# Kernel optimization log

Hardware: AMD Instinct MI355X
Metric: run time of the kernel (lower is better)

Reference implementation:

```python
import jax, jax.numpy as jnp
import numpy as np
import math

B, S, D_MODEL, HEADS, HK = 1024, 81, 64, 4, 16  # S=81 from dim1=5184/64; HK=head dim
FFN, LAYERS, NCLS = 128, 2, 16
EPS = 1e-5


def setup_inputs() -> dict:
    key = jax.random.key(0)
    ks = iter(jax.random.split(key, 40))
    def rn(shape, scale=1.0):
        return jax.random.normal(next(ks), shape, jnp.float32) * scale
    d = {}
    d['X'] = rn((B, 1, 30, 13, 13))
    d['c3w'] = rn((8, 1, 3, 3, 3), 0.1); d['c3b'] = jnp.zeros((8,), jnp.float32)
    d['bn3g'] = jnp.ones((8,), jnp.float32); d['bn3b'] = jnp.zeros((8,), jnp.float32)
    d['c2w'] = rn((64, 224, 3, 3), 0.05); d['c2b'] = jnp.zeros((64,), jnp.float32)
    d['bn2g'] = jnp.ones((64,), jnp.float32); d['bn2b'] = jnp.zeros((64,), jnp.float32)
    d['wq'] = rn((LAYERS, HEADS, D_MODEL, HK), 1.0 / D_MODEL)
    d['wk'] = rn((LAYERS, HEADS, D_MODEL, HK), 1.0 / D_MODEL)
    d['wv'] = rn((LAYERS, HEADS, D_MODEL, HK), 1.0 / D_MODEL)
    d['wg'] = rn((LAYERS, D_MODEL, D_MODEL), 1.0 / D_MODEL)
    d['wo'] = rn((LAYERS, D_MODEL, D_MODEL), 1.0 / D_MODEL)
    d['gng'] = jnp.ones((LAYERS, D_MODEL), jnp.float32); d['gnb'] = jnp.zeros((LAYERS, D_MODEL), jnp.float32)
    d['ln1g'] = jnp.ones((LAYERS, D_MODEL), jnp.float32); d['ln1b'] = jnp.zeros((LAYERS, D_MODEL), jnp.float32)
    d['ln2g'] = jnp.ones((LAYERS, D_MODEL), jnp.float32); d['ln2b'] = jnp.zeros((LAYERS, D_MODEL), jnp.float32)
    d['fw1'] = rn((LAYERS, D_MODEL, FFN), 0.05); d['fb1'] = jnp.zeros((LAYERS, FFN), jnp.float32)
    d['fw2'] = rn((LAYERS, FFN, D_MODEL), 0.05); d['fb2'] = jnp.zeros((LAYERS, D_MODEL), jnp.float32)
    d['nn1w'] = rn((S * D_MODEL, NCLS), 0.02); d['nn1b'] = rn((NCLS,), 1e-6)
    return d


def _bn(x, g, b, axes):
    # BatchNorm in training mode (module default): batch statistics, biased var
    mu = x.mean(axes, keepdims=True)
    var = x.var(axes, keepdims=True)
    shp = [1] * x.ndim; shp[1] = -1
    return (x - mu) / jnp.sqrt(var + EPS) * g.reshape(shp) + b.reshape(shp)


def _ln(x, g, b):
    mu = x.mean(-1, keepdims=True)
    var = x.var(-1, keepdims=True)
    return (x - mu) / jnp.sqrt(var + EPS) * g + b


def _rot2(x):
    # rotate_every_two: (x0,x1,x2,x3,...) -> (-x1,x0,-x3,x2,...)
    x1, x2 = x[..., ::2], x[..., 1::2]
    return jnp.stack((-x2, x1), axis=-1).reshape(x.shape)


def _xpos_tables():
    scale = (jnp.arange(0, HK, 2, dtype=jnp.float32) + 0.4 * HK) / (1.4 * HK)  # (HK/2,)
    pos = jnp.arange(S, dtype=jnp.float32)
    xs = scale[None, :] ** (pos[:, None] / 512.0)                               # (S, HK/2)
    inv_freq = 1.0 / (10000.0 ** (jnp.arange(HK // 2, dtype=jnp.float32) / (HK // 2)))
    ang = pos[:, None] * inv_freq[None, :]
    sin, cos = jnp.sin(ang), jnp.cos(ang)
    dup = lambda m: jnp.repeat(m, 2, axis=-1)                                   # (S, HK)
    return dup(cos * xs), dup(sin * xs), dup(cos / xs), dup(sin / xs)


def _decay_mask():
    g = 1.0 - jnp.exp(jnp.linspace(math.log(1 / 32), math.log(1 / 512), HEADS))
    nm = jnp.arange(S)[:, None] - jnp.arange(S)[None, :]
    return jnp.where(nm >= 0, g[:, None, None] ** nm, 0.0)                      # (H,S,S)


def _forward(X, c3w, c3b, bn3g, bn3b, c2w, c2b, bn2g, bn2b,
             wq, wk, wv, wg, wo, gng, gnb, ln1g, ln1b, ln2g, ln2b,
             fw1, fb1, fw2, fb2, nn1w, nn1b):
    # Convnet front-end
    x = jax.lax.conv_general_dilated(X, c3w, (1, 1, 1), 'VALID',
                                     dimension_numbers=('NCDHW', 'OIDHW', 'NCDHW'))
    x = x + c3b[None, :, None, None, None]
    x = jax.nn.relu(_bn(x, bn3g, bn3b, (0, 2, 3, 4)))        # (B,8,28,11,11)
    x = x.reshape(B, 8 * 28, 11, 11)                           # 'b c h w y -> b (c h) w y'
    x = jax.lax.conv_general_dilated(x, c2w, (1, 1), 'VALID',
                                     dimension_numbers=('NCHW', 'OIHW', 'NCHW'))
    x = x + c2b[None, :, None, None]
    x = jax.nn.relu(_bn(x, bn2g, bn2b, (0, 2, 3)))           # (B,64,9,9)
    x = x.transpose(0, 2, 3, 1).reshape(B, S, D_MODEL)        # 'b c h w -> b (h w) c'

    cu, su, cd, sd = _xpos_tables()
    Dm = _decay_mask()
    for l in range(LAYERS):
        h = _ln(x, ln1g[l], ln1b[l])
        # per-head retention (parallel form)
        Q = jnp.einsum('bsd,hdk->bhsk', h, wq[l])
        K = jnp.einsum('bsd,hdk->bhsk', h, wk[l])
        V = jnp.einsum('bsd,hdk->bhsk', h, wv[l])
        Q = Q * cu + _rot2(Q) * su                            # xpos upscale
        K = K * cd + _rot2(K) * sd                            # xpos downscale
        att = jnp.einsum('bhsk,bhtk->bhst', Q, K) * Dm[None]  # decay-masked scores
        Yh = jnp.einsum('bhst,bhtv->bhsv', att, V)            # (B,H,S,HK)
        # GroupNorm(heads, v_dim) on (B*S, v_dim): per-(b,s,head) normalization
        mu = Yh.mean(-1, keepdims=True)
        var = Yh.var(-1, keepdims=True)
        Yh = (Yh - mu) / jnp.sqrt(var + EPS)
        Yc = Yh.transpose(0, 2, 1, 3).reshape(B, S, D_MODEL) * gng[l] + gnb[l]
        G = h @ wg[l]
        y = (G * jax.nn.sigmoid(G) * Yc) @ wo[l] + x          # swish gate + residual
        h2 = _ln(y, ln2g[l], ln2b[l])
        x = jax.nn.gelu(h2 @ fw1[l] + fb1[l], approximate=False) @ fw2[l] + fb2[l] + y
    return x.reshape(B, S * D_MODEL) @ nn1w + nn1b            # (B, NCLS)


def reference(X, c3w, c3b, bn3g, bn3b, c2w, c2b, bn2g, bn2b,
              wq, wk, wv, wg, wo, gng, gnb, ln1g, ln1b, ln2g, ln2b,
              fw1, fb1, fw2, fb2, nn1w, nn1b):
    return _forward(X, c3w, c3b, bn3g, bn3b, c2w, c2b, bn2g, bn2b,
                    wq, wk, wv, wg, wo, gng, gnb, ln1g, ln1b, ln2g, ln2b,
                    fw1, fb1, fw2, fb2, nn1w, nn1b)
```

## Files before the change

kernel.cpp:

```cpp
#include <hip/hip_runtime.h>
#include <math.h>

#define EPS 1e-5f

#define OFF_A  0u
#define OFF_X0 0u
#define OFF_Y  31850496u
#define OFF_CP 31850496u
#define OFF_WC 32374784u
#define OFF_B  47775744u
#define OFF_P  53084160u
#define OFF_RT 53084160u
#define OFF_ST 53215232u

#define WB_QKV 0u
#define WB_WG  24576u
#define WB_WO  32768u
#define WB_FW1 40960u
#define WB_FW2 57344u

typedef __attribute__((ext_vector_type(8))) short short8;
typedef __attribute__((ext_vector_type(4))) float f32x4;

__device__ inline unsigned short f2bf(float f) {
  unsigned int x = __float_as_uint(f);
  unsigned int r = x + 0x7fffu + ((x >> 16) & 1u);
  return (unsigned short)(r >> 16);
}

__global__ __launch_bounds__(256) void kd1_conv1(const float* X, const float* c3w,
                                                 const float* c3b, float* ws) {
  __shared__ float Xi[5070];
  __shared__ float w3[216];
  int tid = threadIdx.x, b = blockIdx.x;
  for (int u = tid; u < 5070; u += 256) Xi[u] = X[(size_t)b*5070 + u];
  if (tid < 216) w3[tid] = c3w[tid];
  __syncthreads();
  float* Ao = ws + OFF_A + (size_t)b*27104;
  for (int e = tid; e < 27104; e += 256) {
    int pos = e / 224, ci = e - pos*224;
    int o1 = ci / 28, dd = ci - o1*28;
    int h = pos / 11, w = pos - h*11;
    float a = c3b[o1];
    const float* xb = Xi + dd*169 + h*13 + w;
    const float* wp = w3 + o1*27;
#pragma unroll
    for (int kd = 0; kd < 3; ++kd)
#pragma unroll
      for (int kh = 0; kh < 3; ++kh)
#pragma unroll
        for (int kw = 0; kw < 3; ++kw)
          a = fmaf(xb[kd*169 + kh*13 + kw], wp[kd*9 + kh*3 + kw], a);
    Ao[e] = a;
  }
}

__global__ __launch_bounds__(256) void kd2_bn1part(const float* ws_in, float* ws) {
  int b = blockIdx.x, c = threadIdx.x;
  if (c >= 224) return;
  const float* Ab = ws_in + OFF_A + (size_t)b*27104;
  float S = 0.f, Q = 0.f;
  for (int pos = 0; pos < 121; ++pos) {
    float v = Ab[pos*224 + c];
    S += v; Q += v*v;
  }
  ws[OFF_CP + b*448 + c]       = S;
  ws[OFF_CP + b*448 + 224 + c] = Q;
}

__global__ void kd3_bn1fin(const float* ws_in, float* ws,
                           const float* bn3g, const float* bn3b) {
  __shared__ float sS[256], sQ[256];
  int t = threadIdx.x;
  int o1 = t >> 5, j = t & 31;
  float S = 0.f, Q = 0.f;
  for (int b = j; b < 1024; b += 32) {
    const float* P = ws_in + OFF_CP + b*448 + o1*28;
    for (int dd = 0; dd < 28; ++dd) { S += P[dd]; Q += P[224 + dd]; }
  }
  sS[t] = S; sQ[t] = Q;
  __syncthreads();
  if (j == 0) {
    float Ss = 0.f, Qs = 0.f;
    for (int k = 0; k < 32; ++k) { Ss += sS[o1*32 + k]; Qs += sQ[o1*32 + k]; }
    float n = 3469312.f;
    float mean = Ss / n;
    float var = Qs / n - mean*mean;
    float sc = bn3g[o1] * rsqrtf(var + EPS);
    ws[OFF_ST + o1]     = sc;
    ws[OFF_ST + 8 + o1] = bn3b[o1] - mean*sc;
  }
}

__global__ void k0wc(const float* c2w, float* ws) {
  int i = blockIdx.x*256 + threadIdx.x;
  if (i >= 129024) return;
  int ci = i % 224; int r = i / 224; int kpos = r % 9; int oc = r / 9;
  ((unsigned short*)(ws + OFF_WC))[i] = f2bf(c2w[oc*2016 + ci*9 + kpos]);
}

__global__ __launch_bounds__(256) void kd5_conv2_mfma(const float* ws_in, const float* c2b,
                                                      float* ws) {
  __shared__ unsigned short InT[121*232];
  __shared__ float bn1s[224], bn1sh[224];
  const int tid  = threadIdx.x;
  const int b    = blockIdx.x;
  const int wid  = tid >> 6;
  const int lane = tid & 63;
  const int lane15 = lane & 15;
  const int kgrp   = lane >> 4;
  if (tid < 224) {
    int o1 = tid / 28;
    bn1s[tid]  = ws_in[OFF_ST + o1];
    bn1sh[tid] = ws_in[OFF_ST + 8 + o1];
  }
  __syncthreads();
  const float* Ab = ws_in + OFF_A + (size_t)b*27104;
  for (int e = tid; e < 27104; e += 256) {
    int pos = e / 224, ci = e - pos*224;
    float v = fmaxf(bn1s[ci]*Ab[e] + bn1sh[ci], 0.f);
    InT[pos*232 + ci] = f2bf(v);
  }
  __syncthreads();

  int r0[6];
#pragma unroll
  for (int mt = 0; mt < 6; ++mt) {
    int s = mt*16 + lane15; if (s > 80) s = 80;
    int y = s / 9;
    r0[mt] = y*11 + (s - y*9);
  }
  const unsigned short* wcb = (const unsigned short*)(ws_in + OFF_WC);
  const int col = wid*16 + lane15;
  f32x4 acc[6];
#pragma unroll
  for (int mt = 0; mt < 6; ++mt) acc[mt] = (f32x4){0.f,0.f,0.f,0.f};

  for (int kpos = 0; kpos < 9; ++kpos) {
    int ki = kpos / 3, kj = kpos - ki*3;
    int roff = ki*11 + kj;
    const unsigned short* wcp = wcb + ((size_t)col*9 + kpos)*224 + kgrp*8;
#pragma unroll
    for (int Ks = 0; Ks < 7; ++Ks) {
      short8 bf = *(const short8*)(wcp + Ks*32);
#pragma unroll
      for (int mt = 0; mt < 6; ++mt) {
        short8 af = *(const short8*)(InT + (r0[mt] + roff)*232 + Ks*32 + kgrp*8);
        acc[mt] = __builtin_amdgcn_mfma_f32_16x16x32_bf16(af, bf, acc[mt], 0, 0, 0);
      }
    }
  }
  float bias = c2b[col];
  float* Bb = ws + OFF_B + (size_t)b*5184 + col*81;
#pragma unroll
  for (int mt = 0; mt < 6; ++mt) {
#pragma unroll
    for (int r = 0; r < 4; ++r) {
      int s = mt*16 + kgrp*4 + r;
      if (s < 81) Bb[s] = acc[mt][r] + bias;
    }
  }
}

__global__ void kd6_bn2part(const float* ws_in, float* ws) {
  int b = blockIdx.x, t = threadIdx.x;
  const float* Bb = ws_in + OFF_B + (size_t)b * 5184 + t * 81;
  float S = 0.f, Q = 0.f;
  for (int s = 0; s < 81; ++s) {
    float v = Bb[s];
    S += v; Q += v * v;
  }
  ws[OFF_P + b*128 + t]      = S;
  ws[OFF_P + b*128 + 64 + t] = Q;
}

__global__ void kd7_bn2fin(float* ws, const float* bn2g, const float* bn2b) {
  int t = threadIdx.x;
  float S = 0.f, Q = 0.f;
  for (int b = 0; b < 1024; ++b) {
    S += ws[OFF_P + b*128 + t];
    Q += ws[OFF_P + b*128 + 64 + t];
  }
  float n = 82944.f;
  float mean = S / n;
  float var = Q / n - mean * mean;
  float sc = bn2g[t] * rsqrtf(var + EPS);
  ws[OFF_ST + 16 + t] = sc;
  ws[OFF_ST + 80 + t] = bn2b[t] - mean * sc;
}

__global__ void k0rot(float* ws) {
  int i = blockIdx.x * 256 + threadIdx.x;
  if (i >= 1296) return;
  int m = i / 648, r = i - m*648;
  int s = r >> 3, pp = r & 7;
  float scale = (2.f*pp + 6.4f) / 22.4f;
  float xs = powf(scale, (float)s / 512.f);
  float invf = powf(10000.f, -(float)pp / 8.f);
  float ang = (float)s * invf;
  float cx = cosf(ang), sn = sinf(ang);
  float cu = m ? cx/xs : cx*xs;
  float su = m ? sn/xs : sn*xs;
  ws[OFF_RT + i*2]     = cu;
  ws[OFF_RT + i*2 + 1] = su;
}

__global__ __launch_bounds__(256) void kd8_tokens(float* ws) {
  int idx = blockIdx.x * 256 + threadIdx.x;
  if (idx >= 5308416) return;
  int o = idx % 64;
  int s = (idx / 64) % 81;
  int b = idx / 5184;
  float v = ws[OFF_ST + 16 + o] * ws[OFF_B + (size_t)b*5184 + o*81 + s] + ws[OFF_ST + 80 + o];
  ws[OFF_X0 + idx] = fmaxf(v, 0.f);
}

__global__ void k0pack(const float* wq, const float* wk, const float* wv,
                       const float* wg, const float* wo, const float* fw1,
                       const float* fw2, float* ws) {
  int i = blockIdx.x * 256 + threadIdx.x;
  unsigned short* wb = (unsigned short*)(ws + OFF_B);
  if (i < 24576) {
    int l = i / 12288, r = i % 12288;
    int p = r / 6144; r %= 6144;
    int col = r / 64, k = r % 64;
    int m = col >> 5, h2 = (col >> 4) & 1, kk = col & 15;
    const float* src = (m==0) ? wq : (m==1) ? wk : wv;
    wb[i] = f2bf(src[((l*4 + 2*p + h2)*64 + k)*16 + kk]);
  } else if (i < 32768) {
    int j = i - 24576;
    int l = j / 4096, col = (j / 64) & 63, k = j & 63;
    wb[i] = f2bf(wg[(l*64 + k)*64 + col]);
  } else if (i < 40960) {
    int j = i - 32768;
    int l = j / 4096, col = (j / 64) & 63, k = j & 63;
    wb[i] = f2bf(wo[(l*64 + k)*64 + col]);
  } else if (i < 57344) {
    int j = i - 40960;
    int l = j / 8192, col = (j / 64) % 128, k = j & 63;
    wb[i] = f2bf(fw1[(l*64 + k)*128 + col]);
  } else if (i < 73728) {
    int j = i - 57344;
    int l = j / 8192, col = (j / 128) & 63, k = j % 128;
    wb[i] = f2bf(fw2[(l*128 + k)*64 + col]);
  }
}

__global__ __launch_bounds__(256) void fa_layer(const float* ws_in, float* ws,
    const float* ln1g, const float* ln1b, const float* gng, const float* gnb, int l)
{
  __shared__ __align__(16) float sm[15018];
  unsigned short* Hb = (unsigned short*)sm;
  float* P0 = sm + 3840;
  float* P1 = sm + 6594;
  float* P2 = sm + 9348;
  float* P3 = sm + 12102;
  float* XT = sm + 3840;
  unsigned short* Zb = (unsigned short*)(sm + 9348);
  float* muv = sm + 14856;
  float* rsd = sm + 14937;
  const int tid  = threadIdx.x;
  const int b    = blockIdx.x;
  const int wid  = tid >> 6;
  const int lane = tid & 63;
  const int lane15 = lane & 15;
  const int kgrp   = lane >> 4;
  const float* xg = ws_in + OFF_X0 + (size_t)b * 5184;
  const float* rtab = ws_in + OFF_RT;
  const unsigned short* wb = (const unsigned short*)(ws_in + OFF_B);

  for (int u = tid; u < 5184; u += 256) XT[u] = xg[u];
  __syncthreads();
  if (tid < 81) {
    const float* xr = XT + tid*64;
    float sv = 0.f;
    for (int d = 0; d < 64; ++d) sv += xr[d];
    float mean = sv * (1.f/64.f);
    float sq = 0.f;
    for (int d = 0; d < 64; ++d) { float dv = xr[d]-mean; sq += dv*dv; }
    muv[tid] = mean;
    rsd[tid] = rsqrtf(sq*(1.f/64.f) + EPS);
  }
  __syncthreads();
  for (int u = tid; u < 5184; u += 256) {
    int s = u >> 6, d = u & 63;
    Hb[s*80 + d] = f2bf((XT[u] - muv[s])*rsd[s]*ln1g[l*64+d] + ln1b[l*64+d]);
  }
  for (int e = tid; e < 1200; e += 256) Hb[81*80 + e] = 0;
  __syncthreads();

  for (int p = 0; p < 2; ++p) {
    float* QB = p ? P1 : P0;
    float* KB = p ? P2 : P1;
    float* VB = p ? P3 : P2;
    const unsigned short* Bb = wb + WB_QKV + (size_t)(l*2 + p)*6144;
#pragma unroll
    for (int t = 0; t < 3; ++t) {
      int task = wid*3 + t;
      int Nt = task >> 1, mh = task & 1;
      f32x4 acc[3];
#pragma unroll
      for (int m3 = 0; m3 < 3; ++m3) acc[m3] = (f32x4){0.f,0.f,0.f,0.f};
#pragma unroll
      for (int Ks = 0; Ks < 2; ++Ks) {
        short8 bf = *(const short8*)(Bb + (size_t)(Nt*16 + lane15)*64 + Ks*32 + kgrp*8);
#pragma unroll
        for (int m3 = 0; m3 < 3; ++m3) {
          int r = (mh*3 + m3)*16 + lane15;
          short8 af = *(const short8*)(Hb + r*80 + Ks*32 + kgrp*8);
          acc[m3] = __builtin_amdgcn_mfma_f32_16x16x32_bf16(af, bf, acc[m3], 0, 0, 0);
        }
      }
      int col = Nt*16 + lane15;
      int m = col >> 5, idx = col & 31;
      float* dst = (m==0) ? QB : (m==1) ? KB : VB;
#pragma unroll
      for (int m3 = 0; m3 < 3; ++m3) {
#pragma unroll
        for (int r4 = 0; r4 < 4; ++r4) {
          int s = (mh*3 + m3)*16 + kgrp*4 + r4;
          if (s < 81) dst[s*34 + idx] = acc[m3][r4];
        }
      }
    }
    __syncthreads();
    for (int u = tid; u < 2592; u += 256) {
      int m = u / 1296;
      int rem = u - m*1296;
      int h2 = rem / 648;
      int r2 = rem - h2*648;
      int pp = r2 & 7, s = r2 >> 3;
      const float* rt = rtab + (m*648 + s*8 + pp)*2;
      float cu = rt[0], su = rt[1];
      float* ptr = (m ? KB : QB) + s*34 + h2*16 + 2*pp;
      float a = ptr[0], bb2 = ptr[1];
      ptr[0] = a*cu - bb2*su;
      ptr[1] = bb2*cu + a*su;
    }
    __syncthreads();
    if (tid < 162) {
      int h2 = tid & 1, s = tid >> 1;
      int hd = 2*p + h2;
      float g = 1.f - expf(-3.4657359f + (float)hd * (-0.92419624f));
      float lg = log2f(g);
      float q[16];
#pragma unroll
      for (int k = 0; k < 16; ++k) q[k] = QB[s*34 + h2*16 + k];
      float yh[16];
#pragma unroll
      for (int v = 0; v < 16; ++v) yh[v] = 0.f;
      for (int tt = 0; tt <= s; ++tt) {
        const float* Kr = KB + tt*34 + h2*16;
        float a = 0.f;
#pragma unroll
        for (int k = 0; k < 16; ++k) a = fmaf(q[k], Kr[k], a);
        a *= exp2f((float)(s - tt) * lg);
        const float* Vr = VB + tt*34 + h2*16;
#pragma unroll
        for (int v = 0; v < 16; ++v) yh[v] = fmaf(a, Vr[v], yh[v]);
      }
      float sv = 0.f;
#pragma unroll
      for (int v = 0; v < 16; ++v) sv += yh[v];
      float mean = sv * (1.f/16.f);
      float sq = 0.f;
#pragma unroll
      for (int v = 0; v < 16; ++v) { float dv = yh[v]-mean; sq += dv*dv; }
      float rstd = rsqrtf(sq*(1.f/16.f) + EPS);
#pragma unroll
      for (int v = 0; v < 16; ++v) {
        int col = hd*16 + v;
        QB[s*34 + h2*16 + v] = (yh[v]-mean)*rstd*gng[l*64+col] + gnb[l*64+col];
      }
    }
    __syncthreads();
  }

  {
    for (int e = tid; e < 1200; e += 256) Zb[81*80 + e] = 0;
    const unsigned short* Gb = wb + WB_WG + (size_t)l*4096;
    f32x4 acc[6];
#pragma unroll
    for (int mt = 0; mt < 6; ++mt) acc[mt] = (f32x4){0.f,0.f,0.f,0.f};
#pragma unroll
    for (int Ks = 0; Ks < 2; ++Ks) {
      short8 bf = *(const short8*)(Gb + (size_t)(wid*16 + lane15)*64 + Ks*32 + kgrp*8);
#pragma unroll
      for (int mt = 0; mt < 6; ++mt) {
        short8 af = *(const short8*)(Hb + (mt*16 + lane15)*80 + Ks*32 + kgrp*8);
        acc[mt] = __builtin_amdgcn_mfma_f32_16x16x32_bf16(af, bf, acc[mt], 0, 0, 0);
      }
    }
    int col = wid*16 + lane15;
    const float* gnb_ = (col < 32) ? P0 : P1;
#pragma unroll
    for (int mt = 0; mt < 6; ++mt) {
#pragma unroll
      for (int r4 = 0; r4 < 4; ++r4) {
        int s = mt*16 + kgrp*4 + r4;
        if (s < 81) {
          float g = acc[mt][r4];
          float sig = 1.f/(1.f+expf(-g));
          Zb[s*80 + col] = f2bf(g*sig*gnb_[s*34 + (col & 31)]);
        }
      }
    }
  }
  __syncthreads();

  {
    const unsigned short* Ob = wb + WB_WO + (size_t)l*4096;
    float* yg = ws + OFF_Y + (size_t)b * 5184;
    f32x4 acc[6];
#pragma unroll
    for (int mt = 0; mt < 6; ++mt) acc[mt] = (f32x4){0.f,0.f,0.f,0.f};
#pragma unroll
    for (int Ks = 0; Ks < 2; ++Ks) {
      short8 bf = *(const short8*)(Ob + (size_t)(wid*16 + lane15)*64 + Ks*32 + kgrp*8);
#pragma unroll
      for (int mt = 0; mt < 6; ++mt) {
        short8 af = *(const short8*)(Zb + (mt*16 + lane15)*80 + Ks*32 + kgrp*8);
        acc[mt] = __builtin_amdgcn_mfma_f32_16x16x32_bf16(af, bf, acc[mt], 0, 0, 0);
      }
    }
    int col = wid*16 + lane15;
#pragma unroll
    for (int mt = 0; mt < 6; ++mt) {
#pragma unroll
      for (int r4 = 0; r4 < 4; ++r4) {
        int s = mt*16 + kgrp*4 + r4;
        if (s < 81) {
          int u = s*64 + col;
          yg[u] = acc[mt][r4] + xg[u];
        }
      }
    }
  }
}

__global__ __launch_bounds__(256) void ff_layer(const float* ws_in, float* ws,
    const float* fb1, const float* fb2, const float* ln2g, const float* ln2b, int l)
{
  __shared__ __align__(16) float sm[10914];
  unsigned short* H2b = (unsigned short*)sm;
  unsigned short* F1b = (unsigned short*)(sm + 3840);
  float* XT = sm + 3840;
  float* muv = sm + 10752;
  float* rsd = sm + 10833;
  const int tid  = threadIdx.x;
  const int b    = blockIdx.x;
  const int wid  = tid >> 6;
  const int lane = tid & 63;
  const int lane15 = lane & 15;
  const int kgrp   = lane >> 4;
  const float* yg = ws_in + OFF_Y + (size_t)b * 5184;
  const unsigned short* wb = (const unsigned short*)(ws_in + OFF_B);

  for (int u = tid; u < 5184; u += 256) XT[u] = yg[u];
  __syncthreads();
  if (tid < 81) {
    const float* xr = XT + tid*64;
    float sv = 0.f;
    for (int d = 0; d < 64; ++d) sv += xr[d];
    float mean = sv * (1.f/64.f);
    float sq = 0.f;
    for (int d = 0; d < 64; ++d) { float dv = xr[d]-mean; sq += dv*dv; }
    muv[tid] = mean;
    rsd[tid] = rsqrtf(sq*(1.f/64.f) + EPS);
  }
  __syncthreads();
  for (int u = tid; u < 5184; u += 256) {
    int s = u >> 6, d = u & 63;
    H2b[s*80 + d] = f2bf((XT[u] - muv[s])*rsd[s]*ln2g[l*64+d] + ln2b[l*64+d]);
  }
  for (int e = tid; e < 1200; e += 256) H2b[81*80 + e] = 0;
  __syncthreads();

  {
    for (int e = tid; e < 2160; e += 256) F1b[81*144 + e] = 0;
    const unsigned short* Wb1 = wb + WB_FW1 + (size_t)l*8192;
#pragma unroll
    for (int t = 0; t < 4; ++t) {
      int task = wid*4 + t;
      int Nt = task >> 1, mh = task & 1;
      f32x4 acc[3];
#pragma unroll
      for (int m3 = 0; m3 < 3; ++m3) acc[m3] = (f32x4){0.f,0.f,0.f,0.f};
#pragma unroll
      for (int Ks = 0; Ks < 2; ++Ks) {
        short8 bf = *(const short8*)(Wb1 + (size_t)(Nt*16 + lane15)*64 + Ks*32 + kgrp*8);
#pragma unroll
        for (int m3 = 0; m3 < 3; ++m3) {
          int r = (mh*3 + m3)*16 + lane15;
          short8 af = *(const short8*)(H2b + r*80 + Ks*32 + kgrp*8);
          acc[m3] = __builtin_amdgcn_mfma_f32_16x16x32_bf16(af, bf, acc[m3], 0, 0, 0);
        }
      }
      int col = Nt*16 + lane15;
#pragma unroll
      for (int m3 = 0; m3 < 3; ++m3) {
#pragma unroll
        for (int r4 = 0; r4 < 4; ++r4) {
          int s = (mh*3 + m3)*16 + kgrp*4 + r4;
          if (s < 81) {
            float pp = acc[m3][r4] + fb1[l*128 + col];
            F1b[s*144 + col] = f2bf(0.5f*pp*(1.f + erff(pp*0.70710678118f)));
          }
        }
      }
    }
  }
  __syncthreads();

  {
    const unsigned short* Wb2 = wb + WB_FW2 + (size_t)l*8192;
    float* xg = ws + OFF_X0 + (size_t)b * 5184;
    f32x4 acc[6];
#pragma unroll
    for (int mt = 0; mt < 6; ++mt) acc[mt] = (f32x4){0.f,0.f,0.f,0.f};
#pragma unroll
    for (int Ks = 0; Ks < 4; ++Ks) {
      short8 bf = *(const short8*)(Wb2 + (size_t)(wid*16 + lane15)*128 + Ks*32 + kgrp*8);
#pragma unroll
      for (int mt = 0; mt < 6; ++mt) {
        short8 af = *(const short8*)(F1b + (mt*16 + lane15)*144 + Ks*32 + kgrp*8);
        acc[mt] = __builtin_amdgcn_mfma_f32_16x16x32_bf16(af, bf, acc[mt], 0, 0, 0);
      }
    }
    int col = wid*16 + lane15;
#pragma unroll
    for (int mt = 0; mt < 6; ++mt) {
#pragma unroll
      for (int r4 = 0; r4 < 4; ++r4) {
        int s = mt*16 + kgrp*4 + r4;
        if (s < 81) {
          int u = s*64 + col;
          xg[u] = acc[mt][r4] + fb2[l*64 + col] + yg[u];
        }
      }
    }
  }
}

__global__ __launch_bounds__(256) void fcls(const float* ws_in, const float* nn1w,
                                            const float* nn1b, float* out) {
  __shared__ float red[256];
  const int tid = threadIdx.x;
  const int b = blockIdx.x;
  const float* Xr = ws_in + OFF_X0 + (size_t)b * 5184;
  int c = tid & 15, chunk = tid >> 4;
  int i0 = chunk * 324;
  float a = 0.f;
  for (int i = 0; i < 324; ++i)
    a = fmaf(Xr[i0+i], nn1w[(size_t)(i0+i)*16 + c], a);
  red[tid] = a;
  __syncthreads();
  if (tid < 16) {
    float s = nn1b[tid];
#pragma unroll
    for (int j = 0; j < 16; ++j) s += red[j*16 + tid];
    out[b*16 + tid] = s;
  }
}

extern "C" void kernel_launch(void* const* d_in, const int* in_sizes, int n_in,
                              void* d_out, int out_size, void* d_ws, size_t ws_size,
                              hipStream_t stream) {
  const float* X    = (const float*)d_in[0];
  const float* c3w  = (const float*)d_in[1];
  const float* c3b  = (const float*)d_in[2];
  const float* bn3g = (const float*)d_in[3];
  const float* bn3b = (const float*)d_in[4];
  const float* c2w  = (const float*)d_in[5];
  const float* c2b  = (const float*)d_in[6];
  const float* bn2g = (const float*)d_in[7];
  const float* bn2b = (const float*)d_in[8];
  const float* wq   = (const float*)d_in[9];
  const float* wk   = (const float*)d_in[10];
  const float* wv   = (const float*)d_in[11];
  const float* wg   = (const float*)d_in[12];
  const float* wo   = (const float*)d_in[13];
  const float* gng  = (const float*)d_in[14];
  const float* gnb  = (const float*)d_in[15];
  const float* ln1g = (const float*)d_in[16];
  const float* ln1b = (const float*)d_in[17];
  const float* ln2g = (const float*)d_in[18];
  const float* ln2b = (const float*)d_in[19];
  const float* fw1  = (const float*)d_in[20];
  const float* fb1  = (const float*)d_in[21];
  const float* fw2  = (const float*)d_in[22];
  const float* fb2  = (const float*)d_in[23];
  const float* nn1w = (const float*)d_in[24];
  const float* nn1b = (const float*)d_in[25];
  float* ws = (float*)d_ws;
  float* out = (float*)d_out;

  k0wc<<<504, 256, 0, stream>>>(c2w, ws);
  kd1_conv1<<<1024, 256, 0, stream>>>(X, c3w, c3b, ws);
  kd2_bn1part<<<1024, 256, 0, stream>>>(ws, ws);
  kd3_bn1fin<<<1, 256, 0, stream>>>(ws, ws, bn3g, bn3b);
  kd5_conv2_mfma<<<1024, 256, 0, stream>>>(ws, c2b, ws);
  kd6_bn2part<<<1024, 64, 0, stream>>>(ws, ws);
  kd7_bn2fin<<<1, 64, 0, stream>>>(ws, bn2g, bn2b);
  k0rot<<<6, 256, 0, stream>>>(ws);
  kd8_tokens<<<20736, 256, 0, stream>>>(ws);
  k0pack<<<288, 256, 0, stream>>>(wq, wk, wv, wg, wo, fw1, fw2, ws);

  for (int l = 0; l < 2; ++l) {
    fa_layer<<<1024, 256, 0, stream>>>(ws, ws, ln1g, ln1b, gng, gnb, l);
    ff_layer<<<1024, 256, 0, stream>>>(ws, ws, fb1, fb2, ln2g, ln2b, l);
  }

  fcls<<<1024, 256, 0, stream>>>(ws, nn1w, nn1b, out);
}
```

Before: 591.7 us.

## Fuse BN partial stats into conv kernels and store conv1 output as bf16

Folds the BN1 per-channel sum and sum-of-squares into the conv1 kernel and the BN2 partial statistics into the conv2 MFMA epilogue, which removes two launches and two full re-reads of the activations. Conv1 is restructured so each thread owns one channel and slides a register window along w, reusing input taps instead of reloading 27 values per output. The conv1 activation is now written as bf16, halving its write and read traffic. BN1 statistics are still taken from the fp32 values, but conv2 now reads the rounded bf16 copy, adding a small precision loss before the bf16 conversion that already happened. Only 224 of 256 threads do work in conv1.

```diff
diff --git a/kernel.cpp b/kernel.cpp
--- a/kernel.cpp
+++ b/kernel.cpp
@@ -27,6 +27,9 @@
   unsigned int r = x + 0x7fffu + ((x >> 16) & 1u);
   return (unsigned short)(r >> 16);
 }
+__device__ inline float bf2f(unsigned short h) {
+  return __uint_as_float(((unsigned int)h) << 16);
+}
 
 __global__ __launch_bounds__(256) void kd1_conv1(const float* X, const float* c3w,
                                                  const float* c3b, float* ws) {
@@ -36,36 +39,46 @@
   for (int u = tid; u < 5070; u += 256) Xi[u] = X[(size_t)b*5070 + u];
   if (tid < 216) w3[tid] = c3w[tid];
   __syncthreads();
-  float* Ao = ws + OFF_A + (size_t)b*27104;
-  for (int e = tid; e < 27104; e += 256) {
-    int pos = e / 224, ci = e - pos*224;
-    int o1 = ci / 28, dd = ci - o1*28;
-    int h = pos / 11, w = pos - h*11;
-    float a = c3b[o1];
-    const float* xb = Xi + dd*169 + h*13 + w;
-    const float* wp = w3 + o1*27;
-#pragma unroll
-    for (int kd = 0; kd < 3; ++kd)
-#pragma unroll
-      for (int kh = 0; kh < 3; ++kh)
-#pragma unroll
-        for (int kw = 0; kw < 3; ++kw)
-          a = fmaf(xb[kd*169 + kh*13 + kw], wp[kd*9 + kh*3 + kw], a);
-    Ao[e] = a;
-  }
-}
-
-__global__ __launch_bounds__(256) void kd2_bn1part(const float* ws_in, float* ws) {
-  int b = blockIdx.x, c = threadIdx.x;
-  if (c >= 224) return;
-  const float* Ab = ws_in + OFF_A + (size_t)b*27104;
+  if (tid >= 224) return;
+  int o1 = tid / 28, dd = tid - o1*28;
+  float wr[27];
+#pragma unroll
+  for (int k = 0; k < 27; ++k) wr[k] = w3[o1*27 + k];
+  float bias = c3b[o1];
+  unsigned short* Ao = (unsigned short*)(ws + OFF_A) + (size_t)b*27104;
   float S = 0.f, Q = 0.f;
-  for (int pos = 0; pos < 121; ++pos) {
-    float v = Ab[pos*224 + c];
-    S += v; Q += v*v;
-  }
-  ws[OFF_CP + b*448 + c]       = S;
-  ws[OFF_CP + b*448 + 224 + c] = Q;
+  for (int h = 0; h < 11; ++h) {
+    const float* base = Xi + dd*169 + h*13;
+    float c0[9], c1[9], c2[9];
+#pragma unroll
+    for (int j = 0; j < 9; ++j) {
+      int kd = j / 3, kh = j - kd*3;
+      const float* rp = base + kd*169 + kh*13;
+      c0[j] = rp[0]; c1[j] = rp[1]; c2[j] = rp[2];
+    }
+#pragma unroll
+    for (int w = 0; w < 11; ++w) {
+      float a = bias;
+#pragma unroll
+      for (int j = 0; j < 9; ++j) {
+        a = fmaf(c0[j], wr[j*3+0], a);
+        a = fmaf(c1[j], wr[j*3+1], a);
+        a = fmaf(c2[j], wr[j*3+2], a);
+      }
+      Ao[(h*11 + w)*224 + tid] = f2bf(a);
+      S += a; Q += a*a;
+      if (w < 10) {
+#pragma unroll
+        for (int j = 0; j < 9; ++j) {
+          int kd = j / 3, kh = j - kd*3;
+          c0[j] = c1[j]; c1[j] = c2[j];
+          c2[j] = base[kd*169 + kh*13 + w + 3];
+        }
+      }
+    }
+  }
+  ws[OFF_CP + b*448 + tid]       = S;
+  ws[OFF_CP + b*448 + 224 + tid] = Q;
 }
 
 __global__ void kd3_bn1fin(const float* ws_in, float* ws,
@@ -115,10 +128,10 @@
     bn1sh[tid] = ws_in[OFF_ST + 8 + o1];
   }
   __syncthreads();
-  const float* Ab = ws_in + OFF_A + (size_t)b*27104;
+  const unsigned short* Ab = (const unsigned short*)(ws_in + OFF_A) + (size_t)b*27104;
   for (int e = tid; e < 27104; e += 256) {
     int pos = e / 224, ci = e - pos*224;
-    float v = fmaxf(bn1s[ci]*Ab[e] + bn1sh[ci], 0.f);
+    float v = fmaxf(bn1s[ci]*bf2f(Ab[e]) + bn1sh[ci], 0.f);
     InT[pos*232 + ci] = f2bf(v);
   }
   __syncthreads();
@@ -152,26 +165,25 @@
   }
   float bias = c2b[col];
   float* Bb = ws + OFF_B + (size_t)b*5184 + col*81;
+  float S = 0.f, Q = 0.f;
 #pragma unroll
   for (int mt = 0; mt < 6; ++mt) {
 #pragma unroll
     for (int r = 0; r < 4; ++r) {
       int s = mt*16 + kgrp*4 + r;
-      if (s < 81) Bb[s] = acc[mt][r] + bias;
-    }
-  }
-}
-
-__global__ void kd6_bn2part(const float* ws_in, float* ws) {
-  int b = blockIdx.x, t = threadIdx.x;
-  const float* Bb = ws_in + OFF_B + (size_t)b * 5184 + t * 81;
-  float S = 0.f, Q = 0.f;
-  for (int s = 0; s < 81; ++s) {
-    float v = Bb[s];
-    S += v; Q += v * v;
-  }
-  ws[OFF_P + b*128 + t]      = S;
-  ws[OFF_P + b*128 + 64 + t] = Q;
+      if (s < 81) {
+        float v = acc[mt][r] + bias;
+        Bb[s] = v;
+        S += v; Q += v*v;
+      }
+    }
+  }
+  S += __shfl_xor(S, 16); S += __shfl_xor(S, 32);
+  Q += __shfl_xor(Q, 16); Q += __shfl_xor(Q, 32);
+  if (kgrp == 0) {
+    ws[OFF_P + b*128 + col]      = S;
+    ws[OFF_P + b*128 + 64 + col] = Q;
+  }
 }
 
 __global__ void kd7_bn2fin(float* ws, const float* bn2g, const float* bn2b) {
@@ -597,10 +609,8 @@
 
   k0wc<<<504, 256, 0, stream>>>(c2w, ws);
   kd1_conv1<<<1024, 256, 0, stream>>>(X, c3w, c3b, ws);
-  kd2_bn1part<<<1024, 256, 0, stream>>>(ws, ws);
   kd3_bn1fin<<<1, 256, 0, stream>>>(ws, ws, bn3g, bn3b);
   kd5_conv2_mfma<<<1024, 256, 0, stream>>>(ws, c2b, ws);
-  kd6_bn2part<<<1024, 64, 0, stream>>>(ws, ws);
   kd7_bn2fin<<<1, 64, 0, stream>>>(ws, bn2g, bn2b);
   k0rot<<<6, 256, 0, stream>>>(ws);
   kd8_tokens<<<20736, 256, 0, stream>>>(ws);
```

Measured after the change: 532.8 us (median of 4 runs). 10.0% less time.
